# Performance work log

Measured on AMD Instinct MI355X. Metric: run time of the kernel, lower is better.

Reference implementation:

```python
import jax, jax.numpy as jnp
import numpy as np

B, N, IN_DIM, OUT_DIM, H = 8, 1024, 512, 512, 8
SUP = OUT_DIM // H  # support_dim per head = 64


def setup_inputs() -> dict:
    key = jax.random.key(0)
    ks = jax.random.split(key, 6)
    # 0/1 dense adjacency with self-loops so no row is fully masked
    A = jax.random.randint(ks[0], (B, N, N), 0, 2).astype(jnp.float32)
    A = jnp.maximum(A, jnp.eye(N, dtype=jnp.float32)[None])
    X = jax.random.normal(ks[1], (B, N, IN_DIM), dtype=jnp.float32)
    # parameters, uniform(-1/sqrt(fan_last), 1/sqrt(fan_last)) as in reset_parameters
    sw = 1.0 / np.sqrt(SUP)
    W = jax.random.uniform(ks[2], (H, IN_DIM, SUP), minval=-sw, maxval=sw, dtype=jnp.float32)
    w1 = jax.random.uniform(ks[3], (H, SUP), minval=-sw, maxval=sw, dtype=jnp.float32)
    w2 = jax.random.uniform(ks[4], (H, SUP), minval=-sw, maxval=sw, dtype=jnp.float32)
    b = jax.random.uniform(ks[5], (2, H), minval=-1.0, maxval=1.0, dtype=jnp.float32)
    b1, b2 = b[0], b[1]
    return {"A": A, "X": X, "W": W, "w1": w1, "b1": b1, "w2": w2, "b2": b2}


def reference(A, X, W, w1, b1, w2, b2):
    # per-head projection: [B,H,N,SUP]
    inputs = jnp.einsum('bni,hio->bhno', X, W)
    # additive attention logits: self_fc [B,H,N,1] + neigh_fc [B,H,1,N]
    self_fc = jnp.einsum('bhno,ho->bhn', inputs, w1) + b1[None, :, None]
    neigh_fc = jnp.einsum('bhno,ho->bhn', inputs, w2) + b2[None, :, None]
    logits = jax.nn.leaky_relu(self_fc[..., :, None] + neigh_fc[..., None, :], 0.01)
    mask = -1e9 * (1.0 - A)  # [B,N,N]
    alphas = jax.nn.softmax(logits + mask[:, None], axis=-1)  # [B,H,N,N]
    out = jnp.einsum('bhnm,bhmo->bhno', alphas, inputs)
    out = jax.nn.relu(out)  # default activation = torch.relu
    # concat heads on last dim (head i contiguous), matching torch.cat
    return out.transpose(0, 2, 1, 3).reshape(B, N, H * SUP)
```

## Files before the change

### kernel.cpp

```cpp
#include <hip/hip_runtime.h>
#include <hip/hip_fp16.h>

#define BB 8
#define NN 1024
#define IN_DIM 512
#define HH 8
#define SUP 64
#define HS (HH * SUP)

typedef _Float16 half8 __attribute__((ext_vector_type(8)));
typedef _Float16 half4v __attribute__((ext_vector_type(4)));
typedef _Float16 half2v __attribute__((ext_vector_type(2)));
typedef float floatx4 __attribute__((ext_vector_type(4)));

__global__ __launch_bounds__(256) void kprep(const float* __restrict__ A,
                                             unsigned char* __restrict__ Am,
                                             const float* __restrict__ W,
                                             _Float16* __restrict__ Wt,
                                             const float* __restrict__ X,
                                             _Float16* __restrict__ Xh) {
    __shared__ float tile[64][65];
    const int bid = blockIdx.x;
    const int t   = threadIdx.x;
    if (bid < 2048) {
        const int gw   = bid * 4 + (t >> 6);
        const int lane = t & 63;
        const float* arow = A + (size_t)gw * NN;
        unsigned long long keep = 0;
#pragma unroll
        for (int g = 0; g < 16; g++) {
            float a = arow[g * 64 + lane];
            unsigned long long bal = __ballot(a > 0.5f);
            if (lane == g) keep = bal;
        }
        if (lane < 16)
            *(unsigned long long*)(Am + (size_t)gw * 128 + lane * 8) = keep;
    } else if (bid < 2112) {
        const int wb = bid - 2048;
        const int it = wb & 7;
        const int h  = wb >> 3;
        {
            const int i  = t >> 2;
            const int o0 = (t & 3) * 16;
            const float* src = W + ((size_t)h * IN_DIM + it * 64 + i) * SUP + o0;
#pragma unroll
            for (int j = 0; j < 4; j++) {
                float4 v = ((const float4*)src)[j];
                tile[i][o0 + j * 4 + 0] = v.x;
                tile[i][o0 + j * 4 + 1] = v.y;
                tile[i][o0 + j * 4 + 2] = v.z;
                tile[i][o0 + j * 4 + 3] = v.w;
            }
        }
        __syncthreads();
        {
            const int o  = t >> 2;
            const int i0 = (t & 3) * 16;
            _Float16 buf[16];
#pragma unroll
            for (int j = 0; j < 16; j++) buf[j] = (_Float16)tile[i0 + j][o];
            _Float16* dst = Wt + ((size_t)h * SUP + o) * IN_DIM + it * 64 + i0;
            *(half8*)dst       = *(half8*)buf;
            *(half8*)(dst + 8) = *(half8*)(buf + 8);
        }
    } else {
        const int xb = bid - 2112;
#pragma unroll 4
        for (int i = 0; i < 32; i++) {
            const size_t idx = (((size_t)xb * 32 + i) * 256 + t) * 4;
            float4 v = *(const float4*)(X + idx);
            half4v h = {(_Float16)v.x, (_Float16)v.y, (_Float16)v.z, (_Float16)v.w};
            *(half4v*)(Xh + idx) = h;
        }
    }
}

__global__ __launch_bounds__(256) void k1_proj(const _Float16* __restrict__ Xh,
                                               const _Float16* __restrict__ Wt,
                                               const float* __restrict__ w1,
                                               const float* __restrict__ b1,
                                               const float* __restrict__ w2,
                                               const float* __restrict__ b2,
                                               _Float16* __restrict__ Pt,
                                               float* __restrict__ s_g,
                                               float* __restrict__ t_g,
                                               float* __restrict__ tmax16) {
    __shared__ __align__(16) _Float16 xs[2][64 * 40];
    __shared__ __align__(16) _Float16 wsh[2][64 * 40];
    __shared__ __align__(16) _Float16 po[64 * 72];
    __shared__ float tred[64];

    const int bh = blockIdx.y;
    const int b  = bh >> 3;
    const int h  = bh & 7;
    const int n0 = blockIdx.x * 64;
    const int t    = threadIdx.x;
    const int wave = t >> 6;
    const int lane = t & 63;
    const int quad = lane >> 4;
    const int l15  = lane & 15;
    const int row  = t >> 2;
    const int koff = (t & 3) * 8;

    floatx4 acc[4];
#pragma unroll
    for (int i = 0; i < 4; i++) acc[i] = {0.f, 0.f, 0.f, 0.f};

    float w1v[4], w2v[4];
#pragma unroll
    for (int ct = 0; ct < 4; ct++) {
        w1v[ct] = w1[h * 64 + ct * 16 + l15];
        w2v[ct] = w2[h * 64 + ct * 16 + l15];
    }
    const float b1h = b1[h];
    const float b2h = b2[h];

    const _Float16* xbase = Xh + ((size_t)b * NN + n0 + row) * IN_DIM + koff;
    const _Float16* wbase = Wt + ((size_t)h * SUP + row) * IN_DIM + koff;

    half8 xv = *(const half8*)xbase;
    half8 wv = *(const half8*)wbase;

    for (int it = 0; it < 16; it++) {
        const int cur = it & 1;
        *(half8*)&xs[cur][row * 40 + koff]  = xv;
        *(half8*)&wsh[cur][row * 40 + koff] = wv;
        __syncthreads();
        if (it < 15) {
            xv = *(const half8*)(xbase + (it + 1) * 32);
            wv = *(const half8*)(wbase + (it + 1) * 32);
        }
        half8 af = *(const half8*)&xs[cur][(wave * 16 + l15) * 40 + quad * 8];
#pragma unroll
        for (int ct = 0; ct < 4; ct++) {
            half8 bf = *(const half8*)&wsh[cur][(ct * 16 + l15) * 40 + quad * 8];
            acc[ct] = __builtin_amdgcn_mfma_f32_16x16x32_f16(af, bf, acc[ct], 0, 0, 0);
        }
    }
    __syncthreads();

#pragma unroll
    for (int ct = 0; ct < 4; ct++) {
#pragma unroll
        for (int r = 0; r < 4; r++) {
            int o = ct * 16 + l15;
            int n = wave * 16 + quad * 4 + r;
            po[o * 72 + n] = (_Float16)acc[ct][r];
        }
    }
#pragma unroll
    for (int r = 0; r < 4; r++) {
        float sp = 0.f, tp = 0.f;
#pragma unroll
        for (int ct = 0; ct < 4; ct++) {
            sp += acc[ct][r] * w1v[ct];
            tp += acc[ct][r] * w2v[ct];
        }
#pragma unroll
        for (int off = 1; off < 16; off <<= 1) {
            sp += __shfl_xor(sp, off);
            tp += __shfl_xor(tp, off);
        }
        if (l15 == 0) {
            const int n = wave * 16 + quad * 4 + r;
            s_g[(size_t)bh * NN + n0 + n] = sp + b1h;
            float tv = tp + b2h;
            t_g[(size_t)bh * NN + n0 + n] = tv;
            tred[n] = tv;
        }
    }
    __syncthreads();
    {
        const int o   = t >> 2;
        const int nof = (t & 3) * 16;
        _Float16* dst = Pt + ((size_t)bh * SUP + o) * NN + n0 + nof;
        *(half8*)dst       = *(const half8*)&po[o * 72 + nof];
        *(half8*)(dst + 8) = *(const half8*)&po[o * 72 + nof + 8];
    }
    if (t == 0) {
        float m = -1e30f;
#pragma unroll
        for (int i = 0; i < 64; i++) m = fmaxf(m, tred[i]);
        tmax16[bh * 16 + blockIdx.x] = m;
    }
}

__global__ __launch_bounds__(512) void k2_attn(const unsigned char* __restrict__ Am,
                                               const _Float16* __restrict__ Pt,
                                               const float* __restrict__ s_g,
                                               const float* __restrict__ t_g,
                                               const float* __restrict__ tmax16,
                                               float* __restrict__ out) {
    __shared__ __align__(16) _Float16 vts[2][64 * 136];
    __shared__ __align__(16) unsigned t2l[NN / 2];
    __shared__ __align__(16) uint4 lutm[256];

    const int bh = blockIdx.y;
    const int b  = bh >> 3;
    const int h  = bh & 7;
    const int n0 = blockIdx.x * 128;
    const int t    = threadIdx.x;
    const int wave = t >> 6;
    const int lane = t & 63;
    const int quad = lane >> 4;
    const int l15  = lane & 15;
    const int row4 = t >> 3;
    const int seg  = t & 7;

    {
        float2 tv2 = ((const float2*)(t_g + (size_t)bh * NN))[t];
        half2v tp = {(_Float16)tv2.x, (_Float16)tv2.y};
        t2l[t] = *(unsigned*)&tp;
    }
    if (t < 256) {
        unsigned e = (unsigned)t;
        uint4 v;
        v.x = ((e & 1u)   ? 0xFFFFu : 0u) | ((e & 2u)   ? 0xFFFF0000u : 0u);
        v.y = ((e & 4u)   ? 0xFFFFu : 0u) | ((e & 8u)   ? 0xFFFF0000u : 0u);
        v.z = ((e & 16u)  ? 0xFFFFu : 0u) | ((e & 32u)  ? 0xFFFF0000u : 0u);
        v.w = ((e & 64u)  ? 0xFFFFu : 0u) | ((e & 128u) ? 0xFFFF0000u : 0u);
        lutm[t] = v;
    }

    float tmax = -1e30f;
#pragma unroll
    for (int i = 0; i < 16; i++) tmax = fmaxf(tmax, tmax16[bh * 16 + i]);

    const int myrow = wave * 16 + l15;
    const float sv = s_g[(size_t)bh * NN + n0 + myrow];
    const float xc = sv + tmax;
    const float cv = fmaxf(xc, 0.01f * xc);
    const float l2e = 1.44269504f;
    const _Float16 sc1h = (_Float16)((sv - cv) * l2e);
    const _Float16 sc2h = (_Float16)(-0.99f * cv * l2e);
    const half2v sc1 = {sc1h, sc1h};
    const half2v sc2 = {sc2h, sc2h};
    const half2v vl2e = {(_Float16)l2e, (_Float16)l2e};
    const half2v v001 = {(_Float16)0.01f, (_Float16)0.01f};
    const half2v ones2 = {(_Float16)1.0f, (_Float16)1.0f};

    floatx4 acc[4];
#pragma unroll
    for (int i = 0; i < 4; i++) acc[i] = {0.f, 0.f, 0.f, 0.f};
    float zp = 0.f;

    const _Float16* pb = Pt + ((size_t)bh * SUP + row4) * NN + seg * 16;
    half8 v0 = ((const half8*)pb)[0];
    half8 v1 = ((const half8*)pb)[1];
    const uint4* mrow = (const uint4*)(Am + ((size_t)b * NN + n0 + myrow) * 128);
    uint4 mcur = mrow[0];

    for (int mt = 0; mt < 8; mt++) {
        const int cur = mt & 1;
        {
            _Float16* d = &vts[cur][row4 * 136 + seg * 16];
            ((half8*)d)[0] = v0;
            ((half8*)d)[1] = v1;
        }
        __syncthreads();
        uint4 mnext;
        if (mt < 7) {
            const _Float16* p = pb + (mt + 1) * 128;
            v0 = ((const half8*)p)[0];
            v1 = ((const half8*)p)[1];
            mnext = mrow[mt + 1];
        }
        const unsigned mw[4] = {mcur.x, mcur.y, mcur.z, mcur.w};
#pragma unroll
        for (int kk = 0; kk < 4; kk++) {
            const unsigned mbyte = (mw[kk] >> (quad * 8)) & 0xffu;
            uint4 mx = lutm[mbyte];
            const unsigned mxw[4] = {mx.x, mx.y, mx.z, mx.w};
            uint4 tw = *(const uint4*)&t2l[mt * 64 + kk * 16 + quad * 4];
            union { uint4 u; half2v h[4]; } tt; tt.u = tw;
            union { half2v h[4]; half8 h8; } wbu;
#pragma unroll
            for (int p = 0; p < 4; p++) {
                half2v y = tt.h[p] * vl2e + sc1;
                half2v w = y * v001 + sc2;
                half2v z = __builtin_elementwise_max(y, w);
                __half2 zz = *(__half2*)&z;
                __half2 ee = h2exp2(zz);
                unsigned eb = (*(unsigned*)&ee) & mxw[p];
                half2v e2 = *(half2v*)&eb;
#if __has_builtin(__builtin_amdgcn_fdot2)
                zp = __builtin_amdgcn_fdot2(e2, ones2, zp, false);
#else
                zp += (float)e2.x + (float)e2.y;
#endif
                wbu.h[p] = e2;
            }
            half8 af = wbu.h8;
#pragma unroll
            for (int ct = 0; ct < 4; ct++) {
                half8 bf = *(const half8*)&vts[cur][(ct * 16 + l15) * 136 + kk * 32 + quad * 8];
                acc[ct] = __builtin_amdgcn_mfma_f32_16x16x32_f16(af, bf, acc[ct], 0, 0, 0);
            }
        }
        if (mt < 7) mcur = mnext;
    }

    zp += __shfl_xor(zp, 16);
    zp += __shfl_xor(zp, 32);
    const float rzown = 1.0f / zp;

#pragma unroll
    for (int r = 0; r < 4; r++) {
        const int rr = wave * 16 + quad * 4 + r;
        const float rz = __shfl(rzown, quad * 20 + r);
#pragma unroll
        for (int ct = 0; ct < 4; ct++) {
            float v = acc[ct][r] * rz;
            v = v > 0.f ? v : 0.f;
            out[((size_t)b * NN + n0 + rr) * HS + h * SUP + ct * 16 + l15] = v;
        }
    }
}

extern "C" void kernel_launch(void* const* d_in, const int* in_sizes, int n_in,
                              void* d_out, int out_size, void* d_ws, size_t ws_size,
                              hipStream_t stream) {
    const float* A  = (const float*)d_in[0];
    const float* X  = (const float*)d_in[1];
    const float* W  = (const float*)d_in[2];
    const float* w1 = (const float*)d_in[3];
    const float* b1 = (const float*)d_in[4];
    const float* w2 = (const float*)d_in[5];
    const float* b2 = (const float*)d_in[6];
    float* out = (float*)d_out;

    char* ws = (char*)d_ws;
    _Float16*      Wt     = (_Float16*)(ws);
    _Float16*      Pt     = (_Float16*)(ws + 524288);
    float*         s_g    = (float*)(ws + 8912896);
    float*         t_g    = (float*)(ws + 9175040);
    float*         tmax16 = (float*)(ws + 9437184);
    unsigned char* Am     = (unsigned char*)(ws + 9441280);
    _Float16*      Xh     = (_Float16*)(ws + 10489856);

    hipLaunchKernelGGL(kprep, dim3(2048 + 64 + 128), dim3(256), 0, stream, A, Am, W, Wt, X, Xh);
    hipLaunchKernelGGL(k1_proj, dim3(NN / 64, BB * HH), dim3(256), 0, stream,
                       Xh, Wt, w1, b1, w2, b2, Pt, s_g, t_g, tmax16);
    hipLaunchKernelGGL(k2_attn, dim3(NN / 128, BB * HH), dim3(512), 0, stream,
                       Am, Pt, s_g, t_g, tmax16, out);
}
```

Measured before the change: 137.2 us.

## Fuse X conversion and mask build into projection kernel, use expanded halfword mask

Drops the fp16 copy of X. The projection kernel now reads fp32 X directly and converts it while staging to shared memory. The adjacency mask build moves into extra blocks of the projection grid, and the mask is stored as one 16-bit all-ones/zero word per element instead of a packed bitmask. The attention kernel then applies the mask by a direct AND, with no LUT expansion. This removes a separate prep pass and the LUT work, but the mask grows sixteenfold and is re-read by every head. The fp32 X loads are also twice as wide, so memory traffic goes up.

```diff
diff --git a/kernel.cpp b/kernel.cpp
--- a/kernel.cpp
+++ b/kernel.cpp
@@ -9,74 +9,45 @@
 #define HS (HH * SUP)
 
 typedef _Float16 half8 __attribute__((ext_vector_type(8)));
-typedef _Float16 half4v __attribute__((ext_vector_type(4)));
 typedef _Float16 half2v __attribute__((ext_vector_type(2)));
 typedef float floatx4 __attribute__((ext_vector_type(4)));
 
-__global__ __launch_bounds__(256) void kprep(const float* __restrict__ A,
-                                             unsigned char* __restrict__ Am,
-                                             const float* __restrict__ W,
-                                             _Float16* __restrict__ Wt,
-                                             const float* __restrict__ X,
-                                             _Float16* __restrict__ Xh) {
+__global__ __launch_bounds__(256) void kW(const float* __restrict__ W,
+                                          _Float16* __restrict__ Wt) {
     __shared__ float tile[64][65];
-    const int bid = blockIdx.x;
-    const int t   = threadIdx.x;
-    if (bid < 2048) {
-        const int gw   = bid * 4 + (t >> 6);
-        const int lane = t & 63;
-        const float* arow = A + (size_t)gw * NN;
-        unsigned long long keep = 0;
-#pragma unroll
-        for (int g = 0; g < 16; g++) {
-            float a = arow[g * 64 + lane];
-            unsigned long long bal = __ballot(a > 0.5f);
-            if (lane == g) keep = bal;
-        }
-        if (lane < 16)
-            *(unsigned long long*)(Am + (size_t)gw * 128 + lane * 8) = keep;
-    } else if (bid < 2112) {
-        const int wb = bid - 2048;
-        const int it = wb & 7;
-        const int h  = wb >> 3;
-        {
-            const int i  = t >> 2;
-            const int o0 = (t & 3) * 16;
-            const float* src = W + ((size_t)h * IN_DIM + it * 64 + i) * SUP + o0;
-#pragma unroll
-            for (int j = 0; j < 4; j++) {
-                float4 v = ((const float4*)src)[j];
-                tile[i][o0 + j * 4 + 0] = v.x;
-                tile[i][o0 + j * 4 + 1] = v.y;
-                tile[i][o0 + j * 4 + 2] = v.z;
-                tile[i][o0 + j * 4 + 3] = v.w;
-            }
-        }
-        __syncthreads();
-        {
-            const int o  = t >> 2;
-            const int i0 = (t & 3) * 16;
-            _Float16 buf[16];
-#pragma unroll
-            for (int j = 0; j < 16; j++) buf[j] = (_Float16)tile[i0 + j][o];
-            _Float16* dst = Wt + ((size_t)h * SUP + o) * IN_DIM + it * 64 + i0;
-            *(half8*)dst       = *(half8*)buf;
-            *(half8*)(dst + 8) = *(half8*)(buf + 8);
-        }
-    } else {
-        const int xb = bid - 2112;
-#pragma unroll 4
-        for (int i = 0; i < 32; i++) {
-            const size_t idx = (((size_t)xb * 32 + i) * 256 + t) * 4;
-            float4 v = *(const float4*)(X + idx);
-            half4v h = {(_Float16)v.x, (_Float16)v.y, (_Float16)v.z, (_Float16)v.w};
-            *(half4v*)(Xh + idx) = h;
-        }
+    const int it = blockIdx.x & 7;
+    const int h  = blockIdx.x >> 3;
+    const int t  = threadIdx.x;
+    {
+        const int i  = t >> 2;
+        const int o0 = (t & 3) * 16;
+        const float* src = W + ((size_t)h * IN_DIM + it * 64 + i) * SUP + o0;
+#pragma unroll
+        for (int j = 0; j < 4; j++) {
+            float4 v = ((const float4*)src)[j];
+            tile[i][o0 + j * 4 + 0] = v.x;
+            tile[i][o0 + j * 4 + 1] = v.y;
+            tile[i][o0 + j * 4 + 2] = v.z;
+            tile[i][o0 + j * 4 + 3] = v.w;
+        }
+    }
+    __syncthreads();
+    {
+        const int o  = t >> 2;
+        const int i0 = (t & 3) * 16;
+        _Float16 buf[16];
+#pragma unroll
+        for (int j = 0; j < 16; j++) buf[j] = (_Float16)tile[i0 + j][o];
+        _Float16* dst = Wt + ((size_t)h * SUP + o) * IN_DIM + it * 64 + i0;
+        *(half8*)dst       = *(half8*)buf;
+        *(half8*)(dst + 8) = *(half8*)(buf + 8);
     }
 }
 
-__global__ __launch_bounds__(256) void k1_proj(const _Float16* __restrict__ Xh,
+__global__ __launch_bounds__(256) void k1_proj(const float* __restrict__ X,
                                                const _Float16* __restrict__ Wt,
+                                               const float* __restrict__ A,
+                                               unsigned short* __restrict__ Amx,
                                                const float* __restrict__ w1,
                                                const float* __restrict__ b1,
                                                const float* __restrict__ w2,
@@ -90,11 +61,36 @@
     __shared__ __align__(16) _Float16 po[64 * 72];
     __shared__ float tred[64];
 
+    const int t = threadIdx.x;
+
+    if (blockIdx.x >= 16) {
+        const int idx    = (blockIdx.x - 16) * 64 + blockIdx.y;
+        const int row    = idx * 16 + (t >> 4);
+        const int kbase  = (t & 15) * 64;
+        const float* arow = A + (size_t)row * NN + kbase;
+        unsigned short* dst = Amx + (size_t)row * NN + kbase;
+        union { unsigned short s[8]; uint4 u; } pk;
+#pragma unroll
+        for (int g = 0; g < 8; g++) {
+            float4 va = ((const float4*)arow)[g * 2];
+            float4 vb = ((const float4*)arow)[g * 2 + 1];
+            pk.s[0] = va.x > 0.5f ? 0xFFFFu : 0u;
+            pk.s[1] = va.y > 0.5f ? 0xFFFFu : 0u;
+            pk.s[2] = va.z > 0.5f ? 0xFFFFu : 0u;
+            pk.s[3] = va.w > 0.5f ? 0xFFFFu : 0u;
+            pk.s[4] = vb.x > 0.5f ? 0xFFFFu : 0u;
+            pk.s[5] = vb.y > 0.5f ? 0xFFFFu : 0u;
+            pk.s[6] = vb.z > 0.5f ? 0xFFFFu : 0u;
+            pk.s[7] = vb.w > 0.5f ? 0xFFFFu : 0u;
+            *(uint4*)(dst + g * 8) = pk.u;
+        }
+        return;
+    }
+
     const int bh = blockIdx.y;
     const int b  = bh >> 3;
     const int h  = bh & 7;
     const int n0 = blockIdx.x * 64;
-    const int t    = threadIdx.x;
     const int wave = t >> 6;
     const int lane = t & 63;
     const int quad = lane >> 4;
@@ -115,19 +111,26 @@
     const float b1h = b1[h];
     const float b2h = b2[h];
 
-    const _Float16* xbase = Xh + ((size_t)b * NN + n0 + row) * IN_DIM + koff;
+    const float*    xbase = X + ((size_t)b * NN + n0 + row) * IN_DIM + koff;
     const _Float16* wbase = Wt + ((size_t)h * SUP + row) * IN_DIM + koff;
 
-    half8 xv = *(const half8*)xbase;
-    half8 wv = *(const half8*)wbase;
+    float4 xa = ((const float4*)xbase)[0];
+    float4 xb = ((const float4*)xbase)[1];
+    half8  wv = *(const half8*)wbase;
 
     for (int it = 0; it < 16; it++) {
         const int cur = it & 1;
-        *(half8*)&xs[cur][row * 40 + koff]  = xv;
-        *(half8*)&wsh[cur][row * 40 + koff] = wv;
+        {
+            _Float16 xh[8] = {(_Float16)xa.x, (_Float16)xa.y, (_Float16)xa.z, (_Float16)xa.w,
+                              (_Float16)xb.x, (_Float16)xb.y, (_Float16)xb.z, (_Float16)xb.w};
+            *(half8*)&xs[cur][row * 40 + koff]  = *(half8*)xh;
+            *(half8*)&wsh[cur][row * 40 + koff] = wv;
+        }
         __syncthreads();
         if (it < 15) {
-            xv = *(const half8*)(xbase + (it + 1) * 32);
+            const float* src = xbase + (it + 1) * 32;
+            xa = ((const float4*)src)[0];
+            xb = ((const float4*)src)[1];
             wv = *(const half8*)(wbase + (it + 1) * 32);
         }
         half8 af = *(const half8*)&xs[cur][(wave * 16 + l15) * 40 + quad * 8];
@@ -185,7 +188,7 @@
     }
 }
 
-__global__ __launch_bounds__(512) void k2_attn(const unsigned char* __restrict__ Am,
+__global__ __launch_bounds__(512) void k2_attn(const unsigned short* __restrict__ Amx,
                                                const _Float16* __restrict__ Pt,
                                                const float* __restrict__ s_g,
                                                const float* __restrict__ t_g,
@@ -193,7 +196,6 @@
                                                float* __restrict__ out) {
     __shared__ __align__(16) _Float16 vts[2][64 * 136];
     __shared__ __align__(16) unsigned t2l[NN / 2];
-    __shared__ __align__(16) uint4 lutm[256];
 
     const int bh = blockIdx.y;
     const int b  = bh >> 3;
@@ -211,15 +213,6 @@
         float2 tv2 = ((const float2*)(t_g + (size_t)bh * NN))[t];
         half2v tp = {(_Float16)tv2.x, (_Float16)tv2.y};
         t2l[t] = *(unsigned*)&tp;
-    }
-    if (t < 256) {
-        unsigned e = (unsigned)t;
-        uint4 v;
-        v.x = ((e & 1u)   ? 0xFFFFu : 0u) | ((e & 2u)   ? 0xFFFF0000u : 0u);
-        v.y = ((e & 4u)   ? 0xFFFFu : 0u) | ((e & 8u)   ? 0xFFFF0000u : 0u);
-        v.z = ((e & 16u)  ? 0xFFFFu : 0u) | ((e & 32u)  ? 0xFFFF0000u : 0u);
-        v.w = ((e & 64u)  ? 0xFFFFu : 0u) | ((e & 128u) ? 0xFFFF0000u : 0u);
-        lutm[t] = v;
     }
 
     float tmax = -1e30f;
@@ -247,8 +240,11 @@
     const _Float16* pb = Pt + ((size_t)bh * SUP + row4) * NN + seg * 16;
     half8 v0 = ((const half8*)pb)[0];
     half8 v1 = ((const half8*)pb)[1];
-    const uint4* mrow = (const uint4*)(Am + ((size_t)b * NN + n0 + myrow) * 128);
-    uint4 mcur = mrow[0];
+    const unsigned short* mrow = Amx + ((size_t)b * NN + n0 + myrow) * NN + quad * 8;
+    uint4 mk0 = *(const uint4*)(mrow + 0 * 32);
+    uint4 mk1 = *(const uint4*)(mrow + 1 * 32);
+    uint4 mk2 = *(const uint4*)(mrow + 2 * 32);
+    uint4 mk3 = *(const uint4*)(mrow + 3 * 32);
 
     for (int mt = 0; mt < 8; mt++) {
         const int cur = mt & 1;
@@ -258,19 +254,20 @@
             ((half8*)d)[1] = v1;
         }
         __syncthreads();
-        uint4 mnext;
+        uint4 mc[4] = {mk0, mk1, mk2, mk3};
         if (mt < 7) {
             const _Float16* p = pb + (mt + 1) * 128;
             v0 = ((const half8*)p)[0];
             v1 = ((const half8*)p)[1];
-            mnext = mrow[mt + 1];
-        }
-        const unsigned mw[4] = {mcur.x, mcur.y, mcur.z, mcur.w};
+            const unsigned short* mp = mrow + (mt + 1) * 128;
+            mk0 = *(const uint4*)(mp + 0 * 32);
+            mk1 = *(const uint4*)(mp + 1 * 32);
+            mk2 = *(const uint4*)(mp + 2 * 32);
+            mk3 = *(const uint4*)(mp + 3 * 32);
+        }
 #pragma unroll
         for (int kk = 0; kk < 4; kk++) {
-            const unsigned mbyte = (mw[kk] >> (quad * 8)) & 0xffu;
-            uint4 mx = lutm[mbyte];
-            const unsigned mxw[4] = {mx.x, mx.y, mx.z, mx.w};
+            const unsigned mxw[4] = {mc[kk].x, mc[kk].y, mc[kk].z, mc[kk].w};
             uint4 tw = *(const uint4*)&t2l[mt * 64 + kk * 16 + quad * 4];
             union { uint4 u; half2v h[4]; } tt; tt.u = tw;
             union { half2v h[4]; half8 h8; } wbu;
@@ -297,7 +294,6 @@
                 acc[ct] = __builtin_amdgcn_mfma_f32_16x16x32_f16(af, bf, acc[ct], 0, 0, 0);
             }
         }
-        if (mt < 7) mcur = mnext;
     }
 
     zp += __shfl_xor(zp, 16);
@@ -330,17 +326,16 @@
     float* out = (float*)d_out;
 
     char* ws = (char*)d_ws;
-    _Float16*      Wt     = (_Float16*)(ws);
-    _Float16*      Pt     = (_Float16*)(ws + 524288);
-    float*         s_g    = (float*)(ws + 8912896);
-    float*         t_g    = (float*)(ws + 9175040);
-    float*         tmax16 = (float*)(ws + 9437184);
-    unsigned char* Am     = (unsigned char*)(ws + 9441280);
-    _Float16*      Xh     = (_Float16*)(ws + 10489856);
-
-    hipLaunchKernelGGL(kprep, dim3(2048 + 64 + 128), dim3(256), 0, stream, A, Am, W, Wt, X, Xh);
-    hipLaunchKernelGGL(k1_proj, dim3(NN / 64, BB * HH), dim3(256), 0, stream,
-                       Xh, Wt, w1, b1, w2, b2, Pt, s_g, t_g, tmax16);
+    _Float16*       Wt     = (_Float16*)(ws);
+    _Float16*       Pt     = (_Float16*)(ws + 524288);
+    float*          s_g    = (float*)(ws + 8912896);
+    float*          t_g    = (float*)(ws + 9175040);
+    float*          tmax16 = (float*)(ws + 9437184);
+    unsigned short* Amx    = (unsigned short*)(ws + 9441280);
+
+    hipLaunchKernelGGL(kW, dim3(64), dim3(256), 0, stream, W, Wt);
+    hipLaunchKernelGGL(k1_proj, dim3(16 + 8, 64), dim3(256), 0, stream,
+                       X, Wt, A, Amx, w1, b1, w2, b2, Pt, s_g, t_g, tmax16);
     hipLaunchKernelGGL(k2_attn, dim3(NN / 128, BB * HH), dim3(512), 0, stream,
-                       Am, Pt, s_g, t_g, tmax16, out);
+                       Amx, Pt, s_g, t_g, tmax16, out);
 }
```

Result: slower. 143.6 us (+4.7%).

## Fuse X fp16 conversion and adjacency bitmask into projection kernel, two heads per block

Applied to the files above, without the earlier changes.

Removes the separate X-to-fp16 conversion pass: k1_proj now reads fp32 X directly and converts it in registers. Each block computes two heads at once, so every X tile is reused across two heads. The adjacency bitmask packing moves into extra blocks of the projection kernel so it runs alongside the GEMM, leaving a tiny kernel that only transposes W. This cuts the Xh round trip and one serialized prep pass, at the cost of more LDS and registers per projection block and an uneven grid where mask blocks differ from GEMM blocks.

```diff
diff --git a/kernel.cpp b/kernel.cpp
--- a/kernel.cpp
+++ b/kernel.cpp
@@ -9,74 +9,45 @@
 #define HS (HH * SUP)
 
 typedef _Float16 half8 __attribute__((ext_vector_type(8)));
-typedef _Float16 half4v __attribute__((ext_vector_type(4)));
 typedef _Float16 half2v __attribute__((ext_vector_type(2)));
 typedef float floatx4 __attribute__((ext_vector_type(4)));
 
-__global__ __launch_bounds__(256) void kprep(const float* __restrict__ A,
-                                             unsigned char* __restrict__ Am,
-                                             const float* __restrict__ W,
-                                             _Float16* __restrict__ Wt,
-                                             const float* __restrict__ X,
-                                             _Float16* __restrict__ Xh) {
+__global__ __launch_bounds__(256) void kW(const float* __restrict__ W,
+                                          _Float16* __restrict__ Wt) {
     __shared__ float tile[64][65];
-    const int bid = blockIdx.x;
-    const int t   = threadIdx.x;
-    if (bid < 2048) {
-        const int gw   = bid * 4 + (t >> 6);
-        const int lane = t & 63;
-        const float* arow = A + (size_t)gw * NN;
-        unsigned long long keep = 0;
-#pragma unroll
-        for (int g = 0; g < 16; g++) {
-            float a = arow[g * 64 + lane];
-            unsigned long long bal = __ballot(a > 0.5f);
-            if (lane == g) keep = bal;
-        }
-        if (lane < 16)
-            *(unsigned long long*)(Am + (size_t)gw * 128 + lane * 8) = keep;
-    } else if (bid < 2112) {
-        const int wb = bid - 2048;
-        const int it = wb & 7;
-        const int h  = wb >> 3;
-        {
-            const int i  = t >> 2;
-            const int o0 = (t & 3) * 16;
-            const float* src = W + ((size_t)h * IN_DIM + it * 64 + i) * SUP + o0;
-#pragma unroll
-            for (int j = 0; j < 4; j++) {
-                float4 v = ((const float4*)src)[j];
-                tile[i][o0 + j * 4 + 0] = v.x;
-                tile[i][o0 + j * 4 + 1] = v.y;
-                tile[i][o0 + j * 4 + 2] = v.z;
-                tile[i][o0 + j * 4 + 3] = v.w;
-            }
-        }
-        __syncthreads();
-        {
-            const int o  = t >> 2;
-            const int i0 = (t & 3) * 16;
-            _Float16 buf[16];
-#pragma unroll
-            for (int j = 0; j < 16; j++) buf[j] = (_Float16)tile[i0 + j][o];
-            _Float16* dst = Wt + ((size_t)h * SUP + o) * IN_DIM + it * 64 + i0;
-            *(half8*)dst       = *(half8*)buf;
-            *(half8*)(dst + 8) = *(half8*)(buf + 8);
-        }
-    } else {
-        const int xb = bid - 2112;
-#pragma unroll 4
-        for (int i = 0; i < 32; i++) {
-            const size_t idx = (((size_t)xb * 32 + i) * 256 + t) * 4;
-            float4 v = *(const float4*)(X + idx);
-            half4v h = {(_Float16)v.x, (_Float16)v.y, (_Float16)v.z, (_Float16)v.w};
-            *(half4v*)(Xh + idx) = h;
-        }
+    const int it = blockIdx.x & 7;
+    const int h  = blockIdx.x >> 3;
+    const int t  = threadIdx.x;
+    {
+        const int i  = t >> 2;
+        const int o0 = (t & 3) * 16;
+        const float* src = W + ((size_t)h * IN_DIM + it * 64 + i) * SUP + o0;
+#pragma unroll
+        for (int j = 0; j < 4; j++) {
+            float4 v = ((const float4*)src)[j];
+            tile[i][o0 + j * 4 + 0] = v.x;
+            tile[i][o0 + j * 4 + 1] = v.y;
+            tile[i][o0 + j * 4 + 2] = v.z;
+            tile[i][o0 + j * 4 + 3] = v.w;
+        }
+    }
+    __syncthreads();
+    {
+        const int o  = t >> 2;
+        const int i0 = (t & 3) * 16;
+        _Float16 buf[16];
+#pragma unroll
+        for (int j = 0; j < 16; j++) buf[j] = (_Float16)tile[i0 + j][o];
+        _Float16* dst = Wt + ((size_t)h * SUP + o) * IN_DIM + it * 64 + i0;
+        *(half8*)dst       = *(half8*)buf;
+        *(half8*)(dst + 8) = *(half8*)(buf + 8);
     }
 }
 
-__global__ __launch_bounds__(256) void k1_proj(const _Float16* __restrict__ Xh,
+__global__ __launch_bounds__(256) void k1_proj(const float* __restrict__ X,
                                                const _Float16* __restrict__ Wt,
+                                               const float* __restrict__ A,
+                                               unsigned char* __restrict__ Am,
                                                const float* __restrict__ w1,
                                                const float* __restrict__ b1,
                                                const float* __restrict__ w2,
@@ -86,53 +57,86 @@
                                                float* __restrict__ t_g,
                                                float* __restrict__ tmax16) {
     __shared__ __align__(16) _Float16 xs[2][64 * 40];
-    __shared__ __align__(16) _Float16 wsh[2][64 * 40];
-    __shared__ __align__(16) _Float16 po[64 * 72];
-    __shared__ float tred[64];
-
-    const int bh = blockIdx.y;
-    const int b  = bh >> 3;
-    const int h  = bh & 7;
-    const int n0 = blockIdx.x * 64;
+    __shared__ __align__(16) _Float16 wsh[2][128 * 40];
+    __shared__ __align__(16) _Float16 po[128 * 72];
+    __shared__ float tred[2][64];
+
     const int t    = threadIdx.x;
     const int wave = t >> 6;
     const int lane = t & 63;
+
+    if (blockIdx.x >= 16) {
+        const int idx = (blockIdx.x - 16) * 32 + blockIdx.y;
+#pragma unroll
+        for (int i = 0; i < 8; i++) {
+            const int row = idx * 32 + wave * 8 + i;
+            const float* arow = A + (size_t)row * NN;
+            unsigned long long keep = 0;
+#pragma unroll
+            for (int g = 0; g < 16; g++) {
+                float a = arow[g * 64 + lane];
+                unsigned long long bal = __ballot(a > 0.5f);
+                if (lane == g) keep = bal;
+            }
+            if (lane < 16)
+                *(unsigned long long*)(Am + (size_t)row * 128 + lane * 8) = keep;
+        }
+        return;
+    }
+
+    const int bp  = blockIdx.y;
+    const int b   = bp >> 2;
+    const int h0  = (bp & 3) * 2;
+    const int bh0 = b * 8 + h0;
+    const int n0  = blockIdx.x * 64;
     const int quad = lane >> 4;
     const int l15  = lane & 15;
     const int row  = t >> 2;
     const int koff = (t & 3) * 8;
-
-    floatx4 acc[4];
-#pragma unroll
-    for (int i = 0; i < 4; i++) acc[i] = {0.f, 0.f, 0.f, 0.f};
-
-    float w1v[4], w2v[4];
-#pragma unroll
-    for (int ct = 0; ct < 4; ct++) {
-        w1v[ct] = w1[h * 64 + ct * 16 + l15];
-        w2v[ct] = w2[h * 64 + ct * 16 + l15];
-    }
-    const float b1h = b1[h];
-    const float b2h = b2[h];
-
-    const _Float16* xbase = Xh + ((size_t)b * NN + n0 + row) * IN_DIM + koff;
-    const _Float16* wbase = Wt + ((size_t)h * SUP + row) * IN_DIM + koff;
-
-    half8 xv = *(const half8*)xbase;
-    half8 wv = *(const half8*)wbase;
+    const int wrow  = t >> 1;
+    const int wkoff = (t & 1) * 16;
+
+    floatx4 acc[8];
+#pragma unroll
+    for (int i = 0; i < 8; i++) acc[i] = {0.f, 0.f, 0.f, 0.f};
+
+    float w1v[8], w2v[8];
+#pragma unroll
+    for (int ct = 0; ct < 8; ct++) {
+        w1v[ct] = w1[h0 * 64 + ct * 16 + l15];
+        w2v[ct] = w2[h0 * 64 + ct * 16 + l15];
+    }
+    const float b1h0 = b1[h0], b1h1 = b1[h0 + 1];
+    const float b2h0 = b2[h0], b2h1 = b2[h0 + 1];
+
+    const float*    xbase = X + ((size_t)b * NN + n0 + row) * IN_DIM + koff;
+    const _Float16* wbase = Wt + ((size_t)(h0 * SUP) + wrow) * IN_DIM + wkoff;
+
+    float4 xa = ((const float4*)xbase)[0];
+    float4 xb = ((const float4*)xbase)[1];
+    half8  wv0 = ((const half8*)wbase)[0];
+    half8  wv1 = *(const half8*)(wbase + 8);
 
     for (int it = 0; it < 16; it++) {
         const int cur = it & 1;
-        *(half8*)&xs[cur][row * 40 + koff]  = xv;
-        *(half8*)&wsh[cur][row * 40 + koff] = wv;
+        {
+            _Float16 xh[8] = {(_Float16)xa.x, (_Float16)xa.y, (_Float16)xa.z, (_Float16)xa.w,
+                              (_Float16)xb.x, (_Float16)xb.y, (_Float16)xb.z, (_Float16)xb.w};
+            *(half8*)&xs[cur][row * 40 + koff] = *(half8*)xh;
+            *(half8*)&wsh[cur][wrow * 40 + wkoff]     = wv0;
+            *(half8*)&wsh[cur][wrow * 40 + wkoff + 8] = wv1;
+        }
         __syncthreads();
         if (it < 15) {
-            xv = *(const half8*)(xbase + (it + 1) * 32);
-            wv = *(const half8*)(wbase + (it + 1) * 32);
+            const float* src = xbase + (it + 1) * 32;
+            xa = ((const float4*)src)[0];
+            xb = ((const float4*)src)[1];
+            wv0 = *(const half8*)(wbase + (it + 1) * 32);
+            wv1 = *(const half8*)(wbase + (it + 1) * 32 + 8);
         }
         half8 af = *(const half8*)&xs[cur][(wave * 16 + l15) * 40 + quad * 8];
 #pragma unroll
-        for (int ct = 0; ct < 4; ct++) {
+        for (int ct = 0; ct < 8; ct++) {
             half8 bf = *(const half8*)&wsh[cur][(ct * 16 + l15) * 40 + quad * 8];
             acc[ct] = __builtin_amdgcn_mfma_f32_16x16x32_f16(af, bf, acc[ct], 0, 0, 0);
         }
@@ -140,7 +144,7 @@
     __syncthreads();
 
 #pragma unroll
-    for (int ct = 0; ct < 4; ct++) {
+    for (int ct = 0; ct < 8; ct++) {
 #pragma unroll
         for (int r = 0; r < 4; r++) {
             int o = ct * 16 + l15;
@@ -150,38 +154,53 @@
     }
 #pragma unroll
     for (int r = 0; r < 4; r++) {
-        float sp = 0.f, tp = 0.f;
+        float sp0 = 0.f, tp0 = 0.f, sp1 = 0.f, tp1 = 0.f;
 #pragma unroll
         for (int ct = 0; ct < 4; ct++) {
-            sp += acc[ct][r] * w1v[ct];
-            tp += acc[ct][r] * w2v[ct];
+            sp0 += acc[ct][r] * w1v[ct];
+            tp0 += acc[ct][r] * w2v[ct];
+            sp1 += acc[ct + 4][r] * w1v[ct + 4];
+            tp1 += acc[ct + 4][r] * w2v[ct + 4];
         }
 #pragma unroll
         for (int off = 1; off < 16; off <<= 1) {
-            sp += __shfl_xor(sp, off);
-            tp += __shfl_xor(tp, off);
+            sp0 += __shfl_xor(sp0, off);
+            tp0 += __shfl_xor(tp0, off);
+            sp1 += __shfl_xor(sp1, off);
+            tp1 += __shfl_xor(tp1, off);
         }
         if (l15 == 0) {
             const int n = wave * 16 + quad * 4 + r;
-            s_g[(size_t)bh * NN + n0 + n] = sp + b1h;
-            float tv = tp + b2h;
-            t_g[(size_t)bh * NN + n0 + n] = tv;
-            tred[n] = tv;
+            s_g[(size_t)bh0 * NN + n0 + n] = sp0 + b1h0;
+            float tv0 = tp0 + b2h0;
+            t_g[(size_t)bh0 * NN + n0 + n] = tv0;
+            tred[0][n] = tv0;
+            s_g[(size_t)(bh0 + 1) * NN + n0 + n] = sp1 + b1h1;
+            float tv1 = tp1 + b2h1;
+            t_g[(size_t)(bh0 + 1) * NN + n0 + n] = tv1;
+            tred[1][n] = tv1;
         }
     }
     __syncthreads();
     {
-        const int o   = t >> 2;
-        const int nof = (t & 3) * 16;
-        _Float16* dst = Pt + ((size_t)bh * SUP + o) * NN + n0 + nof;
-        *(half8*)dst       = *(const half8*)&po[o * 72 + nof];
-        *(half8*)(dst + 8) = *(const half8*)&po[o * 72 + nof + 8];
+        const int orow = t >> 1;
+        const int nof  = (t & 1) * 32;
+        _Float16* dst = Pt + ((size_t)(bh0 * SUP + orow)) * NN + n0 + nof;
+        const _Float16* src = &po[orow * 72 + nof];
+        *(half8*)dst        = *(const half8*)src;
+        *(half8*)(dst + 8)  = *(const half8*)(src + 8);
+        *(half8*)(dst + 16) = *(const half8*)(src + 16);
+        *(half8*)(dst + 24) = *(const half8*)(src + 24);
     }
     if (t == 0) {
-        float m = -1e30f;
-#pragma unroll
-        for (int i = 0; i < 64; i++) m = fmaxf(m, tred[i]);
-        tmax16[bh * 16 + blockIdx.x] = m;
+        float m0 = -1e30f, m1 = -1e30f;
+#pragma unroll
+        for (int i = 0; i < 64; i++) {
+            m0 = fmaxf(m0, tred[0][i]);
+            m1 = fmaxf(m1, tred[1][i]);
+        }
+        tmax16[bh0 * 16 + blockIdx.x] = m0;
+        tmax16[(bh0 + 1) * 16 + blockIdx.x] = m1;
     }
 }
 
@@ -336,11 +355,10 @@
     float*         t_g    = (float*)(ws + 9175040);
     float*         tmax16 = (float*)(ws + 9437184);
     unsigned char* Am     = (unsigned char*)(ws + 9441280);
-    _Float16*      Xh     = (_Float16*)(ws + 10489856);
-
-    hipLaunchKernelGGL(kprep, dim3(2048 + 64 + 128), dim3(256), 0, stream, A, Am, W, Wt, X, Xh);
-    hipLaunchKernelGGL(k1_proj, dim3(NN / 64, BB * HH), dim3(256), 0, stream,
-                       Xh, Wt, w1, b1, w2, b2, Pt, s_g, t_g, tmax16);
+
+    hipLaunchKernelGGL(kW, dim3(64), dim3(256), 0, stream, W, Wt);
+    hipLaunchKernelGGL(k1_proj, dim3(16 + 8, 32), dim3(256), 0, stream,
+                       X, Wt, A, Am, w1, b1, w2, b2, Pt, s_g, t_g, tmax16);
     hipLaunchKernelGGL(k2_attn, dim3(NN / 128, BB * HH), dim3(512), 0, stream,
                        Am, Pt, s_g, t_g, tmax16, out);
 }
```

New measurement: 133.6 us. 1.03x faster.
